# Kernel tuning notes

Measured on AMD Instinct MI355X. Metric: run time of the kernel, lower is better.

Reference implementation:

```python
import jax, jax.numpy as jnp
import numpy as np


def setup_inputs() -> dict:
    key = jax.random.key(0)
    ks = jax.random.split(key, 9)
    B, C, H, W = 8, 128, 48, 48
    E = C * 6
    s = lambda k, shape, fan_in: jax.random.normal(k, shape, jnp.float32) / np.sqrt(fan_in)
    return {
        "x": jax.random.normal(ks[0], (B, C, H, W), jnp.float32),
        "wq": s(ks[1], (C, C), C), "bq": jnp.zeros((C,), jnp.float32),
        "wk": s(ks[2], (C, C), C), "bk": jnp.zeros((C,), jnp.float32),
        "wv": s(ks[3], (E, C), C), "bv": jnp.zeros((E,), jnp.float32),
        "wo": s(ks[4], (E, E), E), "bo": jnp.zeros((E,), jnp.float32),
    }


def reference(x, wq, bq, wk, bk, wv, bv, wo, bo):
    B, C, H, W = x.shape
    N = H * W
    E = wv.shape[0]
    xf = x.reshape(B, C, N)  # flatten spatial tokens
    # 1x1 convs are channel-wise GEMMs
    q = jnp.einsum('oc,bcn->bno', wq, xf) + bq            # (B, N, C)
    k = jnp.einsum('oc,bcn->bon', wk, xf) + bk[:, None]   # (B, C, N)
    v = jnp.einsum('oc,bcn->bno', wv, xf) + bv            # (B, N, E)
    scale = jnp.asarray(1.0 / np.sqrt(C), x.dtype)
    attn = jax.nn.softmax(jnp.einsum('bnc,bcm->bnm', q, k) * scale, axis=-1)  # (B, N, N)
    out = jnp.einsum('bnm,bme->bne', attn, v)             # (B, N, E)
    out = jnp.einsum('oe,bne->bon', wo, out) + bo[:, None]  # out projection
    return out.reshape(B, E, H, W)
```

## Files before the change

### kernel.cpp

```cpp
#include <hip/hip_runtime.h>
#include <math.h>

constexpr int kB   = 8;
constexpr int kC   = 128;
constexpr int kN   = 2304;
constexpr int kE   = 768;
constexpr int kQKV = kC + kC + kE;

constexpr int TILE = 128;
constexpr int BK   = 32;
constexpr int TPAD = 132;
constexpr int KPAD = 40;

#define SCALE 0.08838834764831845f

typedef float f32x4 __attribute__((ext_vector_type(4)));
typedef short s16x8 __attribute__((ext_vector_type(8)));
typedef short s16x4 __attribute__((ext_vector_type(4)));


__device__ __forceinline__ void load_direct(const float* __restrict__ g, int ld,
                                            int k0, int t0, float (*s)[TPAD]) {
  const int tid = threadIdx.x;
  const int c   = (tid & 31) * 4;
  const int r0  = tid >> 5;
#pragma unroll
  for (int rr = 0; rr < 4; ++rr) {
    const int k = r0 + rr * 8;
    const float4 v = *(const float4*)&g[(size_t)(k0 + k) * ld + t0 + c];
    *(float4*)&s[k][c] = v;
  }
}

__device__ __forceinline__ void load_trans(const float* __restrict__ g, int ld,
                                           int k0, int t0, float (*s)[TPAD]) {
  const int tid = threadIdx.x;
  const int kc  = (tid & 7) * 4;
  const int r0  = tid >> 3;
#pragma unroll
  for (int rr = 0; rr < 4; ++rr) {
    const int t = r0 + rr * 32;
    const float4 v = *(const float4*)&g[(size_t)(t0 + t) * ld + k0 + kc];
    s[kc + 0][t] = v.x;
    s[kc + 1][t] = v.y;
    s[kc + 2][t] = v.z;
    s[kc + 3][t] = v.w;
  }
}

__device__ __forceinline__ void mm_core(const float (*sA)[TPAD], const float (*sB)[TPAD],
                                        int ty, int tx, float acc[2][2][4][4]) {
#pragma unroll
  for (int kk = 0; kk < BK; ++kk) {
    const float4 a0 = *(const float4*)&sA[kk][ty * 4];
    const float4 a1 = *(const float4*)&sA[kk][64 + ty * 4];
    const float4 b0 = *(const float4*)&sB[kk][tx * 4];
    const float4 b1 = *(const float4*)&sB[kk][64 + tx * 4];
    const float a[2][4] = {{a0.x, a0.y, a0.z, a0.w}, {a1.x, a1.y, a1.z, a1.w}};
    const float b[2][4] = {{b0.x, b0.y, b0.z, b0.w}, {b1.x, b1.y, b1.z, b1.w}};
#pragma unroll
    for (int p = 0; p < 2; ++p)
#pragma unroll
      for (int q = 0; q < 2; ++q)
#pragma unroll
        for (int i = 0; i < 4; ++i)
#pragma unroll
          for (int j = 0; j < 4; ++j)
            acc[p][q][i][j] += a[p][i] * b[q][j];
  }
}


__device__ __forceinline__ void split_bf16(float x, unsigned short& hi,
                                           unsigned short& lo) {
  const __bf16 h = (__bf16)x;
  const float  r = x - (float)h;
  const __bf16 l = (__bf16)r;
  hi = __builtin_bit_cast(unsigned short, h);
  lo = __builtin_bit_cast(unsigned short, l);
}

__device__ __forceinline__ void stage_trans_split(
    const float* __restrict__ g, int ld, int k0, int t0,
    unsigned short (*sHi)[KPAD], unsigned short (*sLo)[KPAD]) {
  const int tid = threadIdx.x;
  const int kc  = (tid & 7) * 4;
  const int r0  = tid >> 3;
#pragma unroll
  for (int rr = 0; rr < 4; ++rr) {
    const int t = r0 + rr * 32;
    const float4 v = *(const float4*)&g[(size_t)(t0 + t) * ld + k0 + kc];
    const int kz = kc ^ (((t >> 2) & 3) << 3);
    unsigned short h[4], l[4];
    split_bf16(v.x, h[0], l[0]);
    split_bf16(v.y, h[1], l[1]);
    split_bf16(v.z, h[2], l[2]);
    split_bf16(v.w, h[3], l[3]);
    *(s16x4*)&sHi[t][kz] = (s16x4){(short)h[0], (short)h[1], (short)h[2], (short)h[3]};
    *(s16x4*)&sLo[t][kz] = (s16x4){(short)l[0], (short)l[1], (short)l[2], (short)l[3]};
  }
}

__device__ __forceinline__ void stage_direct_split(
    const float* __restrict__ g, int ld, int k0, int t0,
    unsigned short (*sHi)[KPAD], unsigned short (*sLo)[KPAD]) {
  const int tid = threadIdx.x;
  const int c   = (tid & 31) * 4;
  const int r0  = tid >> 5;
  const int swz = ((c >> 2) & 3) << 3;
#pragma unroll
  for (int rr = 0; rr < 4; ++rr) {
    const int k  = r0 + rr * 8;
    const int kz = k ^ swz;
    const float4 v = *(const float4*)&g[(size_t)(k0 + k) * ld + t0 + c];
    unsigned short h[4], l[4];
    split_bf16(v.x, h[0], l[0]);
    split_bf16(v.y, h[1], l[1]);
    split_bf16(v.z, h[2], l[2]);
    split_bf16(v.w, h[3], l[3]);
#pragma unroll
    for (int u = 0; u < 4; ++u) {
      sHi[c + u][kz] = h[u];
      sLo[c + u][kz] = l[u];
    }
  }
}

__device__ __forceinline__ s16x8 frag8(const unsigned short (*s)[KPAD], int t, int g) {
  const int col = 8 * (g ^ ((t >> 2) & 3));
  return *(const s16x8*)&s[t][col];
}

__device__ __forceinline__ void mfma_core_split(
    const unsigned short (*aHi)[KPAD], const unsigned short (*aLo)[KPAD],
    const unsigned short (*bHi)[KPAD], const unsigned short (*bLo)[KPAD],
    int wr, int wc, int lane, f32x4 acc[4][4]) {
  const int g  = lane >> 4;
  const int tr = lane & 15;
  s16x8 bh[4], bl[4];
#pragma unroll
  for (int ni = 0; ni < 4; ++ni) {
    const int t = wc * 64 + ni * 16 + tr;
    bh[ni] = frag8(bHi, t, g);
    bl[ni] = frag8(bLo, t, g);
  }
#pragma unroll
  for (int mi = 0; mi < 4; ++mi) {
    const int t = wr * 64 + mi * 16 + tr;
    const s16x8 ah = frag8(aHi, t, g);
    const s16x8 al = frag8(aLo, t, g);
#pragma unroll
    for (int ni = 0; ni < 4; ++ni) {
      acc[mi][ni] = __builtin_amdgcn_mfma_f32_16x16x32_bf16(ah, bh[ni], acc[mi][ni], 0, 0, 0);
      acc[mi][ni] = __builtin_amdgcn_mfma_f32_16x16x32_bf16(ah, bl[ni], acc[mi][ni], 0, 0, 0);
      acc[mi][ni] = __builtin_amdgcn_mfma_f32_16x16x32_bf16(al, bh[ni], acc[mi][ni], 0, 0, 0);
    }
  }
}

__global__ __launch_bounds__(256) void qkv_kernel(
    const float* __restrict__ x,
    const float* __restrict__ wq, const float* __restrict__ bq,
    const float* __restrict__ wk, const float* __restrict__ bk,
    const float* __restrict__ wv, const float* __restrict__ bv,
    float* __restrict__ qkv)
{
  __shared__ float sA[BK][TPAD];
  __shared__ float sB[BK][TPAD];
  const int b   = blockIdx.z;
  const int o0  = blockIdx.y * TILE;
  const int n0  = blockIdx.x * TILE;
  const int tid = threadIdx.x;
  const int tx  = tid & 15, ty = tid >> 4;
  float acc[2][2][4][4] = {};
  const float* xb = x + (size_t)b * kC * kN;

  const float* wsrc;
  const float* bsrc;
  int orow0;
  if (o0 < kC)           { wsrc = wq; bsrc = bq; orow0 = o0; }
  else if (o0 < 2 * kC)  { wsrc = wk; bsrc = bk; orow0 = o0 - kC; }
  else                   { wsrc = wv; bsrc = bv; orow0 = o0 - 2 * kC; }

  for (int k0 = 0; k0 < kC; k0 += BK) {
    load_trans(wsrc + (size_t)orow0 * kC, kC, k0, 0, sA);
    load_direct(xb, kN, k0, n0, sB);
    __syncthreads();
    mm_core(sA, sB, ty, tx, acc);
    __syncthreads();
  }

  float* ob = qkv + (size_t)b * kQKV * kN;
#pragma unroll
  for (int p = 0; p < 2; ++p)
#pragma unroll
    for (int i = 0; i < 4; ++i) {
      const int t    = p * 64 + ty * 4 + i;
      const int o    = o0 + t;
      const float bias = bsrc[orow0 + t];
#pragma unroll
      for (int q = 0; q < 2; ++q) {
        float4 r;
        r.x = acc[p][q][i][0] + bias;
        r.y = acc[p][q][i][1] + bias;
        r.z = acc[p][q][i][2] + bias;
        r.w = acc[p][q][i][3] + bias;
        *(float4*)&ob[(size_t)o * kN + n0 + q * 64 + tx * 4] = r;
      }
    }
}

__global__ __launch_bounds__(256) void scores_mfma_kernel(
    const float* __restrict__ qkv, float* __restrict__ scores_slab, int b0)
{
  __shared__ unsigned short sAh[TILE][KPAD], sAl[TILE][KPAD];
  __shared__ unsigned short sBh[TILE][KPAD], sBl[TILE][KPAD];
  const int bz   = blockIdx.z;
  const int n0   = blockIdx.y * TILE;
  const int m0   = blockIdx.x * TILE;
  const int tid  = threadIdx.x;
  const int lane = tid & 63;
  const int wid  = tid >> 6;
  const int wr   = wid >> 1, wc = wid & 1;
  const float* qb = qkv + (size_t)(b0 + bz) * kQKV * kN;
  const float* kb = qb + (size_t)kC * kN;

  f32x4 acc[4][4];
#pragma unroll
  for (int mi = 0; mi < 4; ++mi)
#pragma unroll
    for (int ni = 0; ni < 4; ++ni) acc[mi][ni] = (f32x4)(0.0f);

  for (int k0 = 0; k0 < kC; k0 += BK) {
    stage_direct_split(qb, kN, k0, n0, sAh, sAl);
    stage_direct_split(kb, kN, k0, m0, sBh, sBl);
    __syncthreads();
    mfma_core_split(sAh, sAl, sBh, sBl, wr, wc, lane, acc);
    __syncthreads();
  }

  float* sb = scores_slab + (size_t)bz * kN * kN;
  const int g = lane >> 4, c16 = lane & 15;
#pragma unroll
  for (int mi = 0; mi < 4; ++mi)
#pragma unroll
    for (int ni = 0; ni < 4; ++ni) {
      const int n = n0 + wr * 64 + mi * 16 + 4 * g;
      const int m = m0 + wc * 64 + ni * 16 + c16;
#pragma unroll
      for (int j = 0; j < 4; ++j)
        sb[(size_t)(n + j) * kN + m] = acc[mi][ni][j] * SCALE;
    }
}

__global__ __launch_bounds__(256) void softmax_kernel(float* __restrict__ scores)
{
  const size_t row = blockIdx.x;
  float* p = scores + row * kN;
  const int tid = threadIdx.x;
  float v[9];
  float m = -3.0e38f;
#pragma unroll
  for (int i = 0; i < 9; ++i) {
    v[i] = p[tid + i * 256];
    m = fmaxf(m, v[i]);
  }
#pragma unroll
  for (int off = 32; off >= 1; off >>= 1) m = fmaxf(m, __shfl_down(m, off));
  __shared__ float redm[4], reds[4];
  if ((tid & 63) == 0) redm[tid >> 6] = m;
  __syncthreads();
  m = fmaxf(fmaxf(redm[0], redm[1]), fmaxf(redm[2], redm[3]));
  float s = 0.f;
#pragma unroll
  for (int i = 0; i < 9; ++i) {
    v[i] = expf(v[i] - m);
    s += v[i];
  }
#pragma unroll
  for (int off = 32; off >= 1; off >>= 1) s += __shfl_down(s, off);
  if ((tid & 63) == 0) reds[tid >> 6] = s;
  __syncthreads();
  s = (reds[0] + reds[1]) + (reds[2] + reds[3]);
  const float inv = 1.f / s;
#pragma unroll
  for (int i = 0; i < 9; ++i) p[tid + i * 256] = v[i] * inv;
}

__global__ __launch_bounds__(256) void av_mfma_kernel(
    const float* __restrict__ attn_slab, const float* __restrict__ qkv,
    float* __restrict__ aout, int b0)
{
  __shared__ unsigned short sAh[TILE][KPAD], sAl[TILE][KPAD];
  __shared__ unsigned short sBh[TILE][KPAD], sBl[TILE][KPAD];
  const int bz   = blockIdx.z;
  const int b    = b0 + bz;
  const int n0   = blockIdx.y * TILE;
  const int e0   = blockIdx.x * TILE;
  const int tid  = threadIdx.x;
  const int lane = tid & 63;
  const int wid  = tid >> 6;
  const int wr   = wid >> 1, wc = wid & 1;
  const float* ab = attn_slab + (size_t)bz * kN * kN;
  const float* vb = qkv + (size_t)b * kQKV * kN + (size_t)(2 * kC) * kN;

  f32x4 acc[4][4];
#pragma unroll
  for (int mi = 0; mi < 4; ++mi)
#pragma unroll
    for (int ni = 0; ni < 4; ++ni) acc[mi][ni] = (f32x4)(0.0f);

  for (int k0 = 0; k0 < kN; k0 += BK) {
    stage_trans_split(ab, kN, k0, n0, sAh, sAl);
    stage_trans_split(vb, kN, k0, e0, sBh, sBl);
    __syncthreads();
    mfma_core_split(sAh, sAl, sBh, sBl, wr, wc, lane, acc);
    __syncthreads();
  }

  const int g = lane >> 4, c16 = lane & 15;
#pragma unroll
  for (int mi = 0; mi < 4; ++mi)
#pragma unroll
    for (int ni = 0; ni < 4; ++ni) {
      const int n = n0 + wr * 64 + mi * 16 + 4 * g;
      const int e = e0 + wc * 64 + ni * 16 + c16;
#pragma unroll
      for (int j = 0; j < 4; ++j)
        aout[((size_t)b * kN + n + j) * kE + e] = acc[mi][ni][j];
    }
}

__global__ __launch_bounds__(256) void proj_mfma_kernel(
    const float* __restrict__ wo, const float* __restrict__ bo,
    const float* __restrict__ aout, float* __restrict__ out)
{
  __shared__ unsigned short sAh[TILE][KPAD], sAl[TILE][KPAD];
  __shared__ unsigned short sBh[TILE][KPAD], sBl[TILE][KPAD];
  const int b    = blockIdx.z;
  const int o0   = blockIdx.y * TILE;
  const int n0   = blockIdx.x * TILE;
  const int tid  = threadIdx.x;
  const int lane = tid & 63;
  const int wid  = tid >> 6;
  const int wr   = wid >> 1, wc = wid & 1;
  const float* ob = aout + (size_t)b * kN * kE;

  f32x4 acc[4][4];
#pragma unroll
  for (int mi = 0; mi < 4; ++mi)
#pragma unroll
    for (int ni = 0; ni < 4; ++ni) acc[mi][ni] = (f32x4)(0.0f);

  for (int k0 = 0; k0 < kE; k0 += BK) {
    stage_trans_split(wo, kE, k0, o0, sAh, sAl);
    stage_trans_split(ob, kE, k0, n0, sBh, sBl);
    __syncthreads();
    mfma_core_split(sAh, sAl, sBh, sBl, wr, wc, lane, acc);
    __syncthreads();
  }

  const int g = lane >> 4, c16 = lane & 15;
#pragma unroll
  for (int mi = 0; mi < 4; ++mi)
#pragma unroll
    for (int j = 0; j < 4; ++j) {
      const int o = o0 + wr * 64 + mi * 16 + 4 * g + j;
      const float bias = bo[o];
#pragma unroll
      for (int ni = 0; ni < 4; ++ni) {
        const int n = n0 + wc * 64 + ni * 16 + c16;
        out[((size_t)b * kE + o) * kN + n] = acc[mi][ni][j] + bias;
      }
    }
}

extern "C" void kernel_launch(void* const* d_in, const int* in_sizes, int n_in,
                              void* d_out, int out_size, void* d_ws, size_t ws_size,
                              hipStream_t stream) {
  const float* x  = (const float*)d_in[0];
  const float* wq = (const float*)d_in[1];
  const float* bq = (const float*)d_in[2];
  const float* wk = (const float*)d_in[3];
  const float* bk = (const float*)d_in[4];
  const float* wv = (const float*)d_in[5];
  const float* bv = (const float*)d_in[6];
  const float* wo = (const float*)d_in[7];
  const float* bo = (const float*)d_in[8];
  float* out = (float*)d_out;

  const size_t qkvN   = (size_t)kB * kQKV * kN;
  const size_t slab1  = (size_t)kN * kN;
  const size_t aoutN  = (size_t)kB * kN * kE;
  const size_t baseB  = (qkvN + aoutN) * 4;
  int G = 1;
  if      (ws_size >= baseB + 8 * slab1 * 4) G = 8;
  else if (ws_size >= baseB + 4 * slab1 * 4) G = 4;
  else if (ws_size >= baseB + 2 * slab1 * 4) G = 2;

  float* qkv   = (float*)d_ws;
  float* sslab = qkv + qkvN;
  float* aout  = sslab + (size_t)G * slab1;

  dim3 blk(256);
  qkv_kernel<<<dim3(kN / TILE, kQKV / TILE, kB), blk, 0, stream>>>(
      x, wq, bq, wk, bk, wv, bv, qkv);
  for (int b0 = 0; b0 < kB; b0 += G) {
    scores_mfma_kernel<<<dim3(kN / TILE, kN / TILE, G), blk, 0, stream>>>(
        qkv, sslab, b0);
    softmax_kernel<<<dim3(G * kN), blk, 0, stream>>>(sslab);
    av_mfma_kernel<<<dim3(kE / TILE, kN / TILE, G), blk, 0, stream>>>(
        sslab, qkv, aout, b0);
  }
  proj_mfma_kernel<<<dim3(kN / TILE, kE / TILE, kB), blk, 0, stream>>>(
      wo, bo, aout, out);
}
```

Measured before the change: 649.2 us.

## Store intermediates as pre-split bf16 hi/lo pairs to skip per-tile splitting

Producers (qkv projection, softmax, AV GEMM) now write their outputs as separate bf16 hi and lo halves instead of fp32. A new kernel pre-splits wo the same way. The consuming MFMA kernels then stage tiles with plain vector copies instead of converting fp32 to split bf16 inside every K loop. This removes the repeated split arithmetic, which is redundant because each tile is restaged by many blocks, and it changes the global layouts. The qkv-for-scores path now uses scalar transposed LDS stores, and the batch grouping loop handles a G that does not divide the batch count.

```diff
diff --git a/kernel.cpp b/kernel.cpp
--- a/kernel.cpp
+++ b/kernel.cpp
@@ -12,11 +12,15 @@
 constexpr int TPAD = 132;
 constexpr int KPAD = 40;
 
+constexpr int QROW = 2 * kN;
+constexpr int EROW = 2 * kE;
+
 #define SCALE 0.08838834764831845f
 
-typedef float f32x4 __attribute__((ext_vector_type(4)));
-typedef short s16x8 __attribute__((ext_vector_type(8)));
-typedef short s16x4 __attribute__((ext_vector_type(4)));
+typedef float          f32x4 __attribute__((ext_vector_type(4)));
+typedef short          s16x8 __attribute__((ext_vector_type(8)));
+typedef unsigned short u16x8 __attribute__((ext_vector_type(8)));
+typedef unsigned short u16x4 __attribute__((ext_vector_type(4)));
 
 
 __device__ __forceinline__ void load_direct(const float* __restrict__ g, int ld,
@@ -80,48 +84,42 @@
   lo = __builtin_bit_cast(unsigned short, l);
 }
 
-__device__ __forceinline__ void stage_trans_split(
-    const float* __restrict__ g, int ld, int k0, int t0,
+__device__ __forceinline__ void stage_rows_copy(
+    const unsigned short* __restrict__ base, size_t rstride, int loOff,
     unsigned short (*sHi)[KPAD], unsigned short (*sLo)[KPAD]) {
   const int tid = threadIdx.x;
-  const int kc  = (tid & 7) * 4;
-  const int r0  = tid >> 3;
-#pragma unroll
-  for (int rr = 0; rr < 4; ++rr) {
-    const int t = r0 + rr * 32;
-    const float4 v = *(const float4*)&g[(size_t)(t0 + t) * ld + k0 + kc];
-    const int kz = kc ^ (((t >> 2) & 3) << 3);
-    unsigned short h[4], l[4];
-    split_bf16(v.x, h[0], l[0]);
-    split_bf16(v.y, h[1], l[1]);
-    split_bf16(v.z, h[2], l[2]);
-    split_bf16(v.w, h[3], l[3]);
-    *(s16x4*)&sHi[t][kz] = (s16x4){(short)h[0], (short)h[1], (short)h[2], (short)h[3]};
-    *(s16x4*)&sLo[t][kz] = (s16x4){(short)l[0], (short)l[1], (short)l[2], (short)l[3]};
-  }
-}
-
-__device__ __forceinline__ void stage_direct_split(
-    const float* __restrict__ g, int ld, int k0, int t0,
+  const int t   = tid >> 1;
+  const int h   = tid & 1;
+  const unsigned short* rp = base + (size_t)t * rstride + h * 16;
+  const int sw = ((t >> 2) & 3) << 3;
+  const u16x8 a0 = *(const u16x8*)(rp);
+  const u16x8 a1 = *(const u16x8*)(rp + 8);
+  const u16x8 b0 = *(const u16x8*)(rp + loOff);
+  const u16x8 b1 = *(const u16x8*)(rp + loOff + 8);
+  *(u16x8*)&sHi[t][(h * 16) ^ sw]     = a0;
+  *(u16x8*)&sHi[t][(h * 16 + 8) ^ sw] = a1;
+  *(u16x8*)&sLo[t][(h * 16) ^ sw]     = b0;
+  *(u16x8*)&sLo[t][(h * 16 + 8) ^ sw] = b1;
+}
+
+__device__ __forceinline__ void stage_cols_copy(
+    const unsigned short* __restrict__ base,
     unsigned short (*sHi)[KPAD], unsigned short (*sLo)[KPAD]) {
   const int tid = threadIdx.x;
-  const int c   = (tid & 31) * 4;
-  const int r0  = tid >> 5;
-  const int swz = ((c >> 2) & 3) << 3;
-#pragma unroll
-  for (int rr = 0; rr < 4; ++rr) {
-    const int k  = r0 + rr * 8;
-    const int kz = k ^ swz;
-    const float4 v = *(const float4*)&g[(size_t)(k0 + k) * ld + t0 + c];
-    unsigned short h[4], l[4];
-    split_bf16(v.x, h[0], l[0]);
-    split_bf16(v.y, h[1], l[1]);
-    split_bf16(v.z, h[2], l[2]);
-    split_bf16(v.w, h[3], l[3]);
-#pragma unroll
-    for (int u = 0; u < 4; ++u) {
-      sHi[c + u][kz] = h[u];
-      sLo[c + u][kz] = l[u];
+  const int c   = tid & 31;
+  const int oct = tid >> 5;
+  const unsigned short* rp = base + (size_t)c * QROW;
+#pragma unroll
+  for (int rep = 0; rep < 2; ++rep) {
+    const int nb = oct * 8 + rep * 64;
+    const u16x8 h8 = *(const u16x8*)(rp + nb);
+    const u16x8 l8 = *(const u16x8*)(rp + kN + nb);
+#pragma unroll
+    for (int e = 0; e < 8; ++e) {
+      const int t  = nb + e;
+      const int kz = c ^ (((t >> 2) & 3) << 3);
+      sHi[t][kz] = h8[e];
+      sLo[t][kz] = l8[e];
     }
   }
 }
@@ -158,12 +156,27 @@
   }
 }
 
+__global__ __launch_bounds__(256) void wo_split_kernel(
+    const float* __restrict__ wo, unsigned short* __restrict__ wou)
+{
+  const int o   = blockIdx.x;
+  const int tid = threadIdx.x;
+#pragma unroll
+  for (int i = 0; i < 3; ++i) {
+    const int e = tid + i * 256;
+    unsigned short h, l;
+    split_bf16(wo[(size_t)o * kE + e], h, l);
+    wou[(size_t)o * EROW + e]       = h;
+    wou[(size_t)o * EROW + kE + e]  = l;
+  }
+}
+
 __global__ __launch_bounds__(256) void qkv_kernel(
     const float* __restrict__ x,
     const float* __restrict__ wq, const float* __restrict__ bq,
     const float* __restrict__ wk, const float* __restrict__ bk,
     const float* __restrict__ wv, const float* __restrict__ bv,
-    float* __restrict__ qkv)
+    unsigned short* __restrict__ qkvu)
 {
   __shared__ float sA[BK][TPAD];
   __shared__ float sB[BK][TPAD];
@@ -190,7 +203,6 @@
     __syncthreads();
   }
 
-  float* ob = qkv + (size_t)b * kQKV * kN;
 #pragma unroll
   for (int p = 0; p < 2; ++p)
 #pragma unroll
@@ -198,32 +210,38 @@
       const int t    = p * 64 + ty * 4 + i;
       const int o    = o0 + t;
       const float bias = bsrc[orow0 + t];
+      unsigned short* rowp =
+          qkvu + ((size_t)b * kQKV + o) * QROW + n0;
 #pragma unroll
       for (int q = 0; q < 2; ++q) {
-        float4 r;
-        r.x = acc[p][q][i][0] + bias;
-        r.y = acc[p][q][i][1] + bias;
-        r.z = acc[p][q][i][2] + bias;
-        r.w = acc[p][q][i][3] + bias;
-        *(float4*)&ob[(size_t)o * kN + n0 + q * 64 + tx * 4] = r;
+        u16x4 h4, l4;
+#pragma unroll
+        for (int j = 0; j < 4; ++j) {
+          unsigned short h, l;
+          split_bf16(acc[p][q][i][j] + bias, h, l);
+          h4[j] = h; l4[j] = l;
+        }
+        const int idx = q * 64 + tx * 4;
+        *(u16x4*)&rowp[idx]      = h4;
+        *(u16x4*)&rowp[kN + idx] = l4;
       }
     }
 }
 
 __global__ __launch_bounds__(256) void scores_mfma_kernel(
-    const float* __restrict__ qkv, float* __restrict__ scores_slab, int b0)
+    const unsigned short* __restrict__ qkvu, float* __restrict__ scores_slab,
+    int b0)
 {
   __shared__ unsigned short sAh[TILE][KPAD], sAl[TILE][KPAD];
   __shared__ unsigned short sBh[TILE][KPAD], sBl[TILE][KPAD];
   const int bz   = blockIdx.z;
+  const int b    = b0 + bz;
   const int n0   = blockIdx.y * TILE;
   const int m0   = blockIdx.x * TILE;
   const int tid  = threadIdx.x;
   const int lane = tid & 63;
   const int wid  = tid >> 6;
   const int wr   = wid >> 1, wc = wid & 1;
-  const float* qb = qkv + (size_t)(b0 + bz) * kQKV * kN;
-  const float* kb = qb + (size_t)kC * kN;
 
   f32x4 acc[4][4];
 #pragma unroll
@@ -232,8 +250,8 @@
     for (int ni = 0; ni < 4; ++ni) acc[mi][ni] = (f32x4)(0.0f);
 
   for (int k0 = 0; k0 < kC; k0 += BK) {
-    stage_direct_split(qb, kN, k0, n0, sAh, sAl);
-    stage_direct_split(kb, kN, k0, m0, sBh, sBl);
+    stage_cols_copy(qkvu + ((size_t)b * kQKV + k0) * QROW + n0, sAh, sAl);
+    stage_cols_copy(qkvu + ((size_t)b * kQKV + kC + k0) * QROW + m0, sBh, sBl);
     __syncthreads();
     mfma_core_split(sAh, sAl, sBh, sBl, wr, wc, lane, acc);
     __syncthreads();
@@ -283,13 +301,21 @@
   __syncthreads();
   s = (reds[0] + reds[1]) + (reds[2] + reds[3]);
   const float inv = 1.f / s;
-#pragma unroll
-  for (int i = 0; i < 9; ++i) p[tid + i * 256] = v[i] * inv;
+  unsigned short* pu = (unsigned short*)p;
+#pragma unroll
+  for (int i = 0; i < 9; ++i) {
+    const int idx = tid + i * 256;
+    unsigned short h, l;
+    split_bf16(v[i] * inv, h, l);
+    pu[idx]      = h;
+    pu[kN + idx] = l;
+  }
 }
 
 __global__ __launch_bounds__(256) void av_mfma_kernel(
-    const float* __restrict__ attn_slab, const float* __restrict__ qkv,
-    float* __restrict__ aout, int b0)
+    const unsigned short* __restrict__ pslab,
+    const unsigned short* __restrict__ qkvu,
+    unsigned short* __restrict__ aoutu, int b0)
 {
   __shared__ unsigned short sAh[TILE][KPAD], sAl[TILE][KPAD];
   __shared__ unsigned short sBh[TILE][KPAD], sBl[TILE][KPAD];
@@ -301,8 +327,6 @@
   const int lane = tid & 63;
   const int wid  = tid >> 6;
   const int wr   = wid >> 1, wc = wid & 1;
-  const float* ab = attn_slab + (size_t)bz * kN * kN;
-  const float* vb = qkv + (size_t)b * kQKV * kN + (size_t)(2 * kC) * kN;
 
   f32x4 acc[4][4];
 #pragma unroll
@@ -310,9 +334,12 @@
 #pragma unroll
     for (int ni = 0; ni < 4; ++ni) acc[mi][ni] = (f32x4)(0.0f);
 
+  const unsigned short* pbase = pslab + ((size_t)bz * kN + n0) * QROW;
+  const unsigned short* vbase = qkvu + ((size_t)b * kQKV + 2 * kC + e0) * QROW;
+
   for (int k0 = 0; k0 < kN; k0 += BK) {
-    stage_trans_split(ab, kN, k0, n0, sAh, sAl);
-    stage_trans_split(vb, kN, k0, e0, sBh, sBl);
+    stage_rows_copy(pbase + k0, QROW, kN, sAh, sAl);
+    stage_rows_copy(vbase + k0, QROW, kN, sBh, sBl);
     __syncthreads();
     mfma_core_split(sAh, sAl, sBh, sBl, wr, wc, lane, acc);
     __syncthreads();
@@ -326,14 +353,19 @@
       const int n = n0 + wr * 64 + mi * 16 + 4 * g;
       const int e = e0 + wc * 64 + ni * 16 + c16;
 #pragma unroll
-      for (int j = 0; j < 4; ++j)
-        aout[((size_t)b * kN + n + j) * kE + e] = acc[mi][ni][j];
+      for (int j = 0; j < 4; ++j) {
+        unsigned short h, l;
+        split_bf16(acc[mi][ni][j], h, l);
+        unsigned short* rp = aoutu + ((size_t)b * kN + n + j) * EROW;
+        rp[e]      = h;
+        rp[kE + e] = l;
+      }
     }
 }
 
 __global__ __launch_bounds__(256) void proj_mfma_kernel(
-    const float* __restrict__ wo, const float* __restrict__ bo,
-    const float* __restrict__ aout, float* __restrict__ out)
+    const unsigned short* __restrict__ wou, const float* __restrict__ bo,
+    const unsigned short* __restrict__ aoutu, float* __restrict__ out)
 {
   __shared__ unsigned short sAh[TILE][KPAD], sAl[TILE][KPAD];
   __shared__ unsigned short sBh[TILE][KPAD], sBl[TILE][KPAD];
@@ -344,7 +376,6 @@
   const int lane = tid & 63;
   const int wid  = tid >> 6;
   const int wr   = wid >> 1, wc = wid & 1;
-  const float* ob = aout + (size_t)b * kN * kE;
 
   f32x4 acc[4][4];
 #pragma unroll
@@ -352,9 +383,12 @@
 #pragma unroll
     for (int ni = 0; ni < 4; ++ni) acc[mi][ni] = (f32x4)(0.0f);
 
+  const unsigned short* abase = wou + (size_t)o0 * EROW;
+  const unsigned short* bbase = aoutu + ((size_t)b * kN + n0) * EROW;
+
   for (int k0 = 0; k0 < kE; k0 += BK) {
-    stage_trans_split(wo, kE, k0, o0, sAh, sAl);
-    stage_trans_split(ob, kE, k0, n0, sBh, sBl);
+    stage_rows_copy(abase + k0, EROW, kE, sAh, sAl);
+    stage_rows_copy(bbase + k0, EROW, kE, sBh, sBl);
     __syncthreads();
     mfma_core_split(sAh, sAl, sBh, sBl, wr, wc, lane, acc);
     __syncthreads();
@@ -389,29 +423,33 @@
   const float* bo = (const float*)d_in[8];
   float* out = (float*)d_out;
 
-  const size_t qkvN   = (size_t)kB * kQKV * kN;
-  const size_t slab1  = (size_t)kN * kN;
-  const size_t aoutN  = (size_t)kB * kN * kE;
-  const size_t baseB  = (qkvN + aoutN) * 4;
+  const size_t qkvB  = (size_t)kB * kQKV * QROW * 2;
+  const size_t slab1 = (size_t)kN * kN * 4;
+  const size_t aoutB = (size_t)kB * kN * EROW * 2;
+  const size_t woB   = (size_t)kE * EROW * 2;
+  const size_t baseB = qkvB + aoutB + woB;
   int G = 1;
-  if      (ws_size >= baseB + 8 * slab1 * 4) G = 8;
-  else if (ws_size >= baseB + 4 * slab1 * 4) G = 4;
-  else if (ws_size >= baseB + 2 * slab1 * 4) G = 2;
-
-  float* qkv   = (float*)d_ws;
-  float* sslab = qkv + qkvN;
-  float* aout  = sslab + (size_t)G * slab1;
+  for (int g = 8; g >= 2; --g)
+    if (ws_size >= baseB + (size_t)g * slab1) { G = g; break; }
+
+  char* wsb = (char*)d_ws;
+  unsigned short* qkvu  = (unsigned short*)wsb;
+  float*          sslab = (float*)(wsb + qkvB);
+  unsigned short* aoutu = (unsigned short*)(wsb + qkvB + (size_t)G * slab1);
+  unsigned short* wou   = (unsigned short*)(wsb + qkvB + (size_t)G * slab1 + aoutB);
 
   dim3 blk(256);
+  wo_split_kernel<<<dim3(kE), blk, 0, stream>>>(wo, wou);
   qkv_kernel<<<dim3(kN / TILE, kQKV / TILE, kB), blk, 0, stream>>>(
-      x, wq, bq, wk, bk, wv, bv, qkv);
+      x, wq, bq, wk, bk, wv, bv, qkvu);
   for (int b0 = 0; b0 < kB; b0 += G) {
-    scores_mfma_kernel<<<dim3(kN / TILE, kN / TILE, G), blk, 0, stream>>>(
-        qkv, sslab, b0);
-    softmax_kernel<<<dim3(G * kN), blk, 0, stream>>>(sslab);
-    av_mfma_kernel<<<dim3(kE / TILE, kN / TILE, G), blk, 0, stream>>>(
-        sslab, qkv, aout, b0);
+    const int zz = (kB - b0) < G ? (kB - b0) : G;
+    scores_mfma_kernel<<<dim3(kN / TILE, kN / TILE, zz), blk, 0, stream>>>(
+        qkvu, sslab, b0);
+    softmax_kernel<<<dim3(zz * kN), blk, 0, stream>>>(sslab);
+    av_mfma_kernel<<<dim3(kE / TILE, kN / TILE, zz), blk, 0, stream>>>(
+        (const unsigned short*)sslab, qkvu, aoutu, b0);
   }
   proj_mfma_kernel<<<dim3(kN / TILE, kE / TILE, kB), blk, 0, stream>>>(
-      wo, bo, aout, out);
-}
+      wou, bo, aoutu, out);
+}
```

Result: slower. 681.7 us (+5.0%).
